# Optimization experiments

Hardware: AMD Instinct MI355X
Metric: run time of the kernel (lower is better)

The kernel has to match this reference:

```python
import jax, jax.numpy as jnp
import numpy as np

N = 50000      # num vertices
M = 10000      # num hyperedges
NNZ = 1600000  # incidence list length (avg degree 32)
D = 128        # in_features == out_features


def setup_inputs() -> dict:
    key = jax.random.key(0)
    k0, k1, k2, k3, k4, k5 = jax.random.split(key, 6)
    X = jax.random.normal(k0, (N, D), dtype=jnp.float32)
    X0 = jax.random.normal(k1, (N, D), dtype=jnp.float32)
    vertex = jax.random.randint(k2, (NNZ,), 0, N)
    edges = jax.random.randint(k3, (NNZ,), 0, M)
    # nn.Linear(D, D, bias=False) weight, kaiming-uniform-ish scale
    W = jax.random.uniform(k4, (D, D), dtype=jnp.float32,
                           minval=-1.0, maxval=1.0) / np.float32(np.sqrt(D))
    alpha = jax.random.uniform(k5, (), dtype=jnp.float32)
    beta = jnp.float32(0.5)
    return {"X": X, "X0": X0, "W": W, "alpha": alpha, "beta": beta,
            "vertex": vertex, "edges": edges}


def _scatter_mean(vals, idx, num_segments):
    # segment mean; empty segments -> 0 (matches torch_scatter 'mean')
    s = jax.ops.segment_sum(vals, idx, num_segments=num_segments)
    cnt = jax.ops.segment_sum(jnp.ones(idx.shape, vals.dtype), idx,
                              num_segments=num_segments)
    return s / jnp.maximum(cnt, 1.0)[:, None]


def reference(X, X0, W, alpha, beta, vertex, edges):
    Xve = X[vertex]                          # [NNZ, D] gather vertex -> incidence
    Xe = _scatter_mean(Xve, edges, M)        # [M, D]   hyperedge features
    Xev = Xe[edges]                          # [NNZ, D] gather edge -> incidence
    Xv = _scatter_mean(Xev, vertex, N)       # [N, D]   back to vertices
    Xi = (1.0 - alpha) * Xv + alpha * X0     # initial-residual mix
    return (1.0 - beta) * Xi + beta * (Xi @ W.T)  # identity-map mix + linear
```

## Files before the change

kernel.cpp:

```cpp
#include <hip/hip_runtime.h>
#include <hip/hip_bf16.h>


#define DD 128
#define NV 50000
#define ME 10000

#define CHUNK 4096
#define NEB 157
#define NVB 196
#define PB_CAP 12288

typedef __hip_bfloat16 bf16;
typedef __attribute__((ext_vector_type(8))) short short8v;
typedef __attribute__((ext_vector_type(4))) float float4v;

#define OFF_XE    0
#define OFF_ELIST 2560000
#define OFF_VLIST 8960000
#define OFF_EPAIR 15360000
#define OFF_VPAIR 21760000
#define OFF_XB    15360000
#define OFF_VOFF  28160000
#define OFF_EOFF  28360064
#define OFF_CBH   28400128
#define OFF_GBE   28401664
#define OFF_GBV   28402304
#define OFF_GCE   28403136
#define OFF_GCV   28403776
#define OFF_FLAG  28404608
#define OFF_WF    28404624
#define WS_USED   28470160

__device__ __forceinline__ float bf2f(unsigned short s) {
    union { unsigned u; float f; } x; x.u = ((unsigned)s) << 16; return x.f;
}
__device__ __forceinline__ unsigned f2bfu(float x) {
    union { bf16 h; unsigned short u; } c; c.h = __float2bfloat16(x); return (unsigned)c.u;
}
__device__ __forceinline__ float loadf(const void* p, long long i, unsigned f32) {
    if (f32) return ((const float*)p)[i];
    return bf2f(((const unsigned short*)p)[i]);
}
__device__ __forceinline__ float u2f_lo(unsigned x) {
    union { unsigned u; float f; } c; c.u = x << 16; return c.f;
}
__device__ __forceinline__ float u2f_hi(unsigned x) {
    union { unsigned u; float f; } c; c.u = x & 0xFFFF0000u; return c.f;
}
__device__ __forceinline__ void acc8(const uint4& u, float* a) {
    a[0] += u2f_lo(u.x); a[1] += u2f_hi(u.x);
    a[2] += u2f_lo(u.y); a[3] += u2f_hi(u.y);
    a[4] += u2f_lo(u.z); a[5] += u2f_hi(u.z);
    a[6] += u2f_lo(u.w); a[7] += u2f_hi(u.w);
}

__device__ __forceinline__ unsigned wave_is_fp32(const unsigned short* p) {
    int l = threadIdx.x & 63;
    int big = 0;
    for (int i = l; i < 256; i += 64) {
        unsigned e = (p[i] >> 7) & 0xFFu;
        if (e >= 0x90u) big++;
    }
    for (int s = 32; s > 0; s >>= 1) big += __shfl_down(big, s);
    return (__shfl(big, 0) >= 4) ? 1u : 0u;
}

__global__ __launch_bounds__(256) void prep_all(const void* X, const void* X0, const void* W,
                                                const void* beta_p,
                                                const int* __restrict__ vertex,
                                                const int* __restrict__ edges,
                                                unsigned* __restrict__ flags,
                                                unsigned short* __restrict__ Wfrag,
                                                unsigned* __restrict__ cbh, int nnz) {
    __shared__ unsigned h[NEB + NVB];
    int b = blockIdx.x, t = threadIdx.x;

    if (b == 0) {
        if (t < 64) {
            const unsigned short* px[3] = {(const unsigned short*)X,
                                           (const unsigned short*)X0,
                                           (const unsigned short*)W};
            for (int k = 0; k < 3; k++) {
                int big = 0;
                for (int i = t; i < 256; i += 64) {
                    unsigned e = (px[k][i] >> 7) & 0xFFu;
                    if (e >= 0x90u) big++;
                }
                for (int s = 32; s > 0; s >>= 1) big += __shfl_down(big, s);
                if (t == 0) flags[k] = (big >= 4) ? 1u : 0u;
            }
            if (t == 0) {
                unsigned short bb = *(const unsigned short*)beta_p;
                flags[3] = (bb == 0x3F00u) ? 0u : 1u;
            }
        }
        return;
    }

    if (b <= 8) {
        int blob = (b - 1) * 256 + t;
        unsigned fW = wave_is_fp32((const unsigned short*)W);
        unsigned short bu = *(const unsigned short*)beta_p;
        unsigned fS = (bu == 0x3F00u) ? 0u : 1u;
        int lane = blob & 63, kk = (blob >> 6) & 3, ct = blob >> 8;
        int nn = lane & 15, quad = lane >> 4;
        int c = ct * 16 + nn;
        int kbase = kk * 32 + quad * 8;
        float beta = loadf(beta_p, 0, fS);
        float omb = 1.f - beta;
        unsigned short hi[8], lo[8];
#pragma unroll
        for (int j = 0; j < 8; j++) {
            float wv = loadf(W, (long long)c * DD + kbase + j, fW);
            float v = beta * wv + ((kbase + j) == c ? omb : 0.f);
            unsigned short hh = (unsigned short)f2bfu(v);
            hi[j] = hh;
            lo[j] = (unsigned short)f2bfu(v - bf2f(hh));
        }
        uint4 ph, pl;
        ph.x = (unsigned)hi[0] | ((unsigned)hi[1] << 16);
        ph.y = (unsigned)hi[2] | ((unsigned)hi[3] << 16);
        ph.z = (unsigned)hi[4] | ((unsigned)hi[5] << 16);
        ph.w = (unsigned)hi[6] | ((unsigned)hi[7] << 16);
        pl.x = (unsigned)lo[0] | ((unsigned)lo[1] << 16);
        pl.y = (unsigned)lo[2] | ((unsigned)lo[3] << 16);
        pl.z = (unsigned)lo[4] | ((unsigned)lo[5] << 16);
        pl.w = (unsigned)lo[6] | ((unsigned)lo[7] << 16);
        ((uint4*)Wfrag)[blob] = ph;
        ((uint4*)Wfrag)[2048 + blob] = pl;
        return;
    }

    int hb = b - 9;
    for (int i = t; i < NEB + NVB; i += 256) h[i] = 0;
    __syncthreads();
    int stride = 512 * 256;
    for (int i = hb * 256 + t; i < nnz; i += stride) {
        atomicAdd(&h[edges[i] >> 6], 1u);
        atomicAdd(&h[NEB + (vertex[i] >> 8)], 1u);
    }
    __syncthreads();
    for (int i = t; i < NEB + NVB; i += 256) {
        unsigned v = h[i];
        if (v) atomicAdd(&cbh[i], v);
    }
}

__global__ __launch_bounds__(256) void conv_x(const void* __restrict__ X,
                                              unsigned short* __restrict__ Xb,
                                              const unsigned* __restrict__ flags) {
    if (!flags[0]) return;
    int i = blockIdx.x * 256 + threadIdx.x;
    if (i >= NV * DD / 8) return;
    const float4* p = (const float4*)X + (size_t)i * 2;
    float4 a = p[0], b = p[1];
    uint4 o;
    o.x = f2bfu(a.x) | (f2bfu(a.y) << 16);
    o.y = f2bfu(a.z) | (f2bfu(a.w) << 16);
    o.z = f2bfu(b.x) | (f2bfu(b.y) << 16);
    o.w = f2bfu(b.z) | (f2bfu(b.w) << 16);
    ((uint4*)Xb)[i] = o;
}

__global__ void scan353(const unsigned* __restrict__ cbh,
                        unsigned* __restrict__ gbe, unsigned* __restrict__ gbv,
                        unsigned* __restrict__ gce, unsigned* __restrict__ gcv,
                        unsigned* __restrict__ voff, unsigned* __restrict__ eoff,
                        int nnz) {
    __shared__ unsigned s[512];
    int t = threadIdx.x;
    unsigned v = (t < NEB + NVB) ? cbh[t] : 0u;
    s[t] = v;
    __syncthreads();
    for (int st = 1; st < 512; st <<= 1) {
        unsigned u = (t >= st) ? s[t - st] : 0u;
        __syncthreads();
        s[t] += u;
        __syncthreads();
    }
    unsigned excl = s[t] - v;
    if (t < NEB) {
        gbe[t] = excl; gce[t] = excl;
    } else if (t < NEB + NVB) {
        unsigned base = s[NEB - 1];
        gbv[t - NEB] = excl - base;
        gcv[t - NEB] = excl - base;
    }
    if (t == 0) {
        gbe[NEB] = (unsigned)nnz;
        gbv[NVB] = (unsigned)nnz;
        eoff[ME] = (unsigned)nnz;
        voff[NV] = (unsigned)nnz;
    }
}

__global__ __launch_bounds__(256) void build_pairs(const int* __restrict__ vertex,
                                                   const int* __restrict__ edges,
                                                   unsigned* __restrict__ gcur_e,
                                                   unsigned* __restrict__ gcur_v,
                                                   unsigned* __restrict__ epairs,
                                                   unsigned* __restrict__ vpairs, int nnz) {
    __shared__ unsigned buf[CHUNK];
    __shared__ unsigned hist[256], scn[256], loff[256], cur[256], gbase[256];
    int t = threadIdx.x;
    int base = blockIdx.x * CHUNK;
    int len = min(CHUNK, nnz - base);
    if (len <= 0) return;

    unsigned pkr[16];

    hist[t] = 0;
    __syncthreads();
#pragma unroll
    for (int it = 0; it < 16; it++) {
        int i = t + it * 256;
        if (i < len) {
            unsigned e = (unsigned)edges[base + i];
            unsigned v = (unsigned)vertex[base + i];
            unsigned pk = (e << 16) | v;
            pkr[it] = pk;
            atomicAdd(&hist[pk >> 22], 1u);
        }
    }
    __syncthreads();
    unsigned hv = hist[t];
    scn[t] = hv;
    __syncthreads();
    for (int st = 1; st < 256; st <<= 1) {
        unsigned u = (t >= st) ? scn[t - st] : 0u;
        __syncthreads();
        scn[t] += u;
        __syncthreads();
    }
    loff[t] = scn[t] - hv;
    cur[t] = scn[t] - hv;
    if (t < NEB && hv > 0) gbase[t] = atomicAdd(&gcur_e[t], hv);
    __syncthreads();
#pragma unroll
    for (int it = 0; it < 16; it++) {
        int i = t + it * 256;
        if (i < len) {
            unsigned pk = pkr[it];
            unsigned p = atomicAdd(&cur[pk >> 22], 1u);
            buf[p] = pk;
        }
    }
    __syncthreads();
    for (int i = t; i < len; i += 256) {
        unsigned pk = buf[i];
        unsigned b = pk >> 22;
        epairs[gbase[b] + (i - loff[b])] = pk;
    }

    __syncthreads();
    hist[t] = 0;
    __syncthreads();
#pragma unroll
    for (int it = 0; it < 16; it++) {
        int i = t + it * 256;
        if (i < len) {
            unsigned pk = buf[i];
            unsigned npk = (pk << 16) | (pk >> 16);
            pkr[it] = npk;
            atomicAdd(&hist[npk >> 24], 1u);
        }
    }
    __syncthreads();
    hv = hist[t];
    scn[t] = hv;
    __syncthreads();
    for (int st = 1; st < 256; st <<= 1) {
        unsigned u = (t >= st) ? scn[t - st] : 0u;
        __syncthreads();
        scn[t] += u;
        __syncthreads();
    }
    loff[t] = scn[t] - hv;
    cur[t] = scn[t] - hv;
    if (t < NVB && hv > 0) gbase[t] = atomicAdd(&gcur_v[t], hv);
    __syncthreads();
#pragma unroll
    for (int it = 0; it < 16; it++) {
        int i = t + it * 256;
        if (i < len) {
            unsigned npk = pkr[it];
            unsigned p = atomicAdd(&cur[npk >> 24], 1u);
            buf[p] = npk;
        }
    }
    __syncthreads();
    for (int i = t; i < len; i += 256) {
        unsigned npk = buf[i];
        unsigned b = npk >> 24;
        vpairs[gbase[b] + (i - loff[b])] = npk;
    }
}

__global__ __launch_bounds__(256) void build_lists(const unsigned* __restrict__ epairs,
                                                   const unsigned* __restrict__ vpairs,
                                                   const unsigned* __restrict__ gbe,
                                                   const unsigned* __restrict__ gbv,
                                                   unsigned* __restrict__ eoff,
                                                   unsigned* __restrict__ voff,
                                                   unsigned* __restrict__ elist,
                                                   unsigned* __restrict__ vlist) {
    __shared__ unsigned buf[PB_CAP];
    __shared__ unsigned offs[256], curs[256];
    int b = blockIdx.x, t = threadIdx.x;
    const unsigned* pairs;
    unsigned* off;
    unsigned* list;
    unsigned s0, s1;
    int k0, nk;
    if (b < NEB) {
        pairs = epairs; off = eoff; list = elist;
        k0 = b << 6; nk = min(64, ME - k0);
        s0 = gbe[b]; s1 = gbe[b + 1];
    } else {
        int bb = b - NEB;
        pairs = vpairs; off = voff; list = vlist;
        k0 = bb << 8; nk = min(256, NV - k0);
        s0 = gbv[bb]; s1 = gbv[bb + 1];
    }
    int len = (int)(s1 - s0);

    curs[t] = 0;
    __syncthreads();
    for (int i = t; i < len; i += 256) {
        unsigned pk = pairs[s0 + i];
        atomicAdd(&curs[(pk >> 16) - k0], 1u);
    }
    __syncthreads();
    unsigned hv = curs[t];
    offs[t] = hv;
    __syncthreads();
    for (int st = 1; st < 256; st <<= 1) {
        unsigned u = (t >= st) ? offs[t - st] : 0u;
        __syncthreads();
        offs[t] += u;
        __syncthreads();
    }
    unsigned my_excl = offs[t] - hv;
    __syncthreads();
    offs[t] = my_excl;
    curs[t] = 0;
    if (t < nk) off[k0 + t] = s0 + my_excl;
    __syncthreads();

    if (len <= PB_CAP) {
        for (int i = t; i < len; i += 256) {
            unsigned pk = pairs[s0 + i];
            int lk = (int)(pk >> 16) - k0;
            unsigned p = offs[lk] + atomicAdd(&curs[lk], 1u);
            buf[p] = pk & 0xFFFFu;
        }
        __syncthreads();
        for (int i = t; i < len; i += 256) list[s0 + i] = buf[i];
    } else {
        for (int i = t; i < len; i += 256) {
            unsigned pk = pairs[s0 + i];
            int lk = (int)(pk >> 16) - k0;
            unsigned p = offs[lk] + atomicAdd(&curs[lk], 1u);
            list[s0 + p] = pk & 0xFFFFu;
        }
    }
}

__global__ __launch_bounds__(256, 8) void edge_agg(const void* __restrict__ X,
                                                   const unsigned short* __restrict__ Xb,
                                                   const unsigned* __restrict__ eoff,
                                                   const unsigned* __restrict__ elist,
                                                   unsigned short* __restrict__ Xe,
                                                   const unsigned* __restrict__ flags, int m) {
    __shared__ float red[4][DD];
    int e = blockIdx.x;
    int t = threadIdx.x, lane = t & 63, w = t >> 6;
    const unsigned short* Xp = flags[0] ? Xb : (const unsigned short*)X;
    unsigned s0 = eoff[e], s1 = eoff[e + 1];
    float a[8];
#pragma unroll
    for (int i = 0; i < 8; i++) a[i] = 0.f;

    int sub = t & 15;
    unsigned q = s0 + (unsigned)(t >> 4);
    for (; q + 48 < s1; q += 64) {
        unsigned v0 = elist[q], v1 = elist[q + 16];
        unsigned v2 = elist[q + 32], v3 = elist[q + 48];
        uint4 u0 = *(const uint4*)(Xp + (size_t)v0 * DD + 8 * sub);
        uint4 u1 = *(const uint4*)(Xp + (size_t)v1 * DD + 8 * sub);
        uint4 u2 = *(const uint4*)(Xp + (size_t)v2 * DD + 8 * sub);
        uint4 u3 = *(const uint4*)(Xp + (size_t)v3 * DD + 8 * sub);
        acc8(u0, a); acc8(u1, a); acc8(u2, a); acc8(u3, a);
    }
    for (; q + 16 < s1; q += 32) {
        unsigned v0 = elist[q], v1 = elist[q + 16];
        uint4 u0 = *(const uint4*)(Xp + (size_t)v0 * DD + 8 * sub);
        uint4 u1 = *(const uint4*)(Xp + (size_t)v1 * DD + 8 * sub);
        acc8(u0, a); acc8(u1, a);
    }
    if (q < s1) {
        unsigned v0 = elist[q];
        uint4 u0 = *(const uint4*)(Xp + (size_t)v0 * DD + 8 * sub);
        acc8(u0, a);
    }
#pragma unroll
    for (int i = 0; i < 8; i++) {
        a[i] += __shfl_xor(a[i], 16);
        a[i] += __shfl_xor(a[i], 32);
    }
    if ((lane >> 4) == 0) {
#pragma unroll
        for (int i = 0; i < 8; i++) red[w][8 * sub + i] = a[i];
    }
    __syncthreads();
    if (t < DD) {
        float inv = (s1 > s0) ? 1.f / (float)(s1 - s0) : 1.f;
        float v = (red[0][t] + red[1][t] + red[2][t] + red[3][t]) * inv;
        Xe[(size_t)e * DD + t] = (unsigned short)f2bfu(v);
    }
}

__global__ __launch_bounds__(256, 8) void vertex_out(const unsigned short* __restrict__ Xe,
                                                     const unsigned* __restrict__ voff,
                                                     const unsigned* __restrict__ vlist,
                                                     const void* __restrict__ X0,
                                                     const unsigned short* __restrict__ Wfrag,
                                                     const void* __restrict__ alpha_p,
                                                     void* __restrict__ out,
                                                     const unsigned* __restrict__ flags, int n) {
    __shared__ short8v A_hi[272];
    __shared__ short8v A_lo[272];
    int t = threadIdx.x, lane = t & 63, w = t >> 6;
    unsigned fX = flags[0], f0 = flags[1], fS = flags[3];
    float alpha = loadf(alpha_p, 0, fS);
    float oma = 1.f - alpha;
    int v0 = blockIdx.x * 16;

    int g = lane >> 4, sub = lane & 15;
    for (int j = 0; j < 4; j++) {
        int r = w * 4 + j, v = v0 + r;
        int idx = (sub >> 2) * 68 + (sub & 3) * 17 + r;
        float a[8];
#pragma unroll
        for (int i = 0; i < 8; i++) a[i] = 0.f;
        if (v < n) {
            unsigned s0 = voff[v], s1 = voff[v + 1];
            unsigned q = s0;
            for (; q + 8 <= s1; q += 8) {
                unsigned e0 = vlist[q + g];
                unsigned e1 = vlist[q + 4 + g];
                uint4 u0 = *(const uint4*)(Xe + (size_t)e0 * DD + 8 * sub);
                uint4 u1 = *(const uint4*)(Xe + (size_t)e1 * DD + 8 * sub);
                acc8(u0, a); acc8(u1, a);
            }
            if (q + 4 <= s1) {
                unsigned e0 = vlist[q + g];
                uint4 u0 = *(const uint4*)(Xe + (size_t)e0 * DD + 8 * sub);
                acc8(u0, a);
                q += 4;
            }
            int rem = (int)(s1 - q);
            if (g < rem) {
                unsigned e0 = vlist[q + g];
                uint4 u0 = *(const uint4*)(Xe + (size_t)e0 * DD + 8 * sub);
                acc8(u0, a);
            }
#pragma unroll
            for (int i = 0; i < 8; i++) {
                a[i] += __shfl_xor(a[i], 16);
                a[i] += __shfl_xor(a[i], 32);
            }
            if (g == 0) {
                float inv = (s1 > s0) ? 1.f / (float)(s1 - s0) : 1.f;
                float x0[8];
                if (!f0) {
                    uint4 xu = *(const uint4*)((const unsigned short*)X0 + (size_t)v * DD + 8 * sub);
                    x0[0] = u2f_lo(xu.x); x0[1] = u2f_hi(xu.x);
                    x0[2] = u2f_lo(xu.y); x0[3] = u2f_hi(xu.y);
                    x0[4] = u2f_lo(xu.z); x0[5] = u2f_hi(xu.z);
                    x0[6] = u2f_lo(xu.w); x0[7] = u2f_hi(xu.w);
                } else {
                    const float4* p = (const float4*)((const float*)X0 + (size_t)v * DD + 8 * sub);
                    float4 xA = p[0], xB = p[1];
                    x0[0] = xA.x; x0[1] = xA.y; x0[2] = xA.z; x0[3] = xA.w;
                    x0[4] = xB.x; x0[5] = xB.y; x0[6] = xB.z; x0[7] = xB.w;
                }
                short8v ah, al;
#pragma unroll
                for (int i = 0; i < 8; i++) {
                    float xi = oma * (a[i] * inv) + alpha * x0[i];
                    unsigned short hh = (unsigned short)f2bfu(xi);
                    ah[i] = (short)hh;
                    al[i] = (short)f2bfu(xi - bf2f(hh));
                }
                A_hi[idx] = ah;
                A_lo[idx] = al;
            }
        } else if (g == 0) {
            short8v zf = {0, 0, 0, 0, 0, 0, 0, 0};
            A_hi[idx] = zf;
            A_lo[idx] = zf;
        }
    }

    __syncthreads();
    int ct = w;
    short8v ah[4], al[4];
#pragma unroll
    for (int kk = 0; kk < 4; kk++) {
        int ridx = kk * 68 + (lane >> 4) * 17 + (lane & 15);
        ah[kk] = A_hi[ridx];
        al[kk] = A_lo[ridx];
    }
    const short8v* Bh = (const short8v*)Wfrag;
    const short8v* Bl = Bh + 2048;
#pragma unroll
    for (int tt = 0; tt < 2; tt++) {
        int c2 = ct + 4 * tt;
        float4v acc = {0.f, 0.f, 0.f, 0.f};
#pragma unroll
        for (int kk = 0; kk < 4; kk++) {
            short8v bh = Bh[(c2 * 4 + kk) * 64 + lane];
            short8v bl = Bl[(c2 * 4 + kk) * 64 + lane];
            acc = __builtin_amdgcn_mfma_f32_16x16x32_bf16(ah[kk], bh, acc, 0, 0, 0);
            acc = __builtin_amdgcn_mfma_f32_16x16x32_bf16(al[kk], bh, acc, 0, 0, 0);
            acc = __builtin_amdgcn_mfma_f32_16x16x32_bf16(ah[kk], bl, acc, 0, 0, 0);
        }
        int col = c2 * 16 + (lane & 15);
        int rbase = v0 + (lane >> 4) * 4;
#pragma unroll
        for (int reg = 0; reg < 4; reg++) {
            int row = rbase + reg;
            if (row < n) {
                if (fX) ((float*)out)[(size_t)row * DD + col] = acc[reg];
                else    ((bf16*)out)[(size_t)row * DD + col] = __float2bfloat16(acc[reg]);
            }
        }
    }
}

extern "C" void kernel_launch(void* const* d_in, const int* in_sizes, int n_in,
                              void* d_out, int out_size, void* d_ws, size_t ws_size,
                              hipStream_t stream) {
    const void* X      = d_in[0];
    const void* X0     = d_in[1];
    const void* W      = d_in[2];
    const void* alpha  = d_in[3];
    const void* beta   = d_in[4];
    const int*  vertex = (const int*)d_in[5];
    const int*  edges  = (const int*)d_in[6];
    const int nnz = in_sizes[5];

    char* ws = (char*)d_ws;
    unsigned short* Xe = (unsigned short*)(ws + OFF_XE);
    unsigned* elist  = (unsigned*)(ws + OFF_ELIST);
    unsigned* vlist  = (unsigned*)(ws + OFF_VLIST);
    unsigned* epairs = (unsigned*)(ws + OFF_EPAIR);
    unsigned* vpairs = (unsigned*)(ws + OFF_VPAIR);
    unsigned short* Xb = (unsigned short*)(ws + OFF_XB);
    unsigned* voff   = (unsigned*)(ws + OFF_VOFF);
    unsigned* eoff   = (unsigned*)(ws + OFF_EOFF);
    unsigned* cbh    = (unsigned*)(ws + OFF_CBH);
    unsigned* gbe    = (unsigned*)(ws + OFF_GBE);
    unsigned* gbv    = (unsigned*)(ws + OFF_GBV);
    unsigned* gce    = (unsigned*)(ws + OFF_GCE);
    unsigned* gcv    = (unsigned*)(ws + OFF_GCV);
    unsigned* flags  = (unsigned*)(ws + OFF_FLAG);
    unsigned short* Wfrag = (unsigned short*)(ws + OFF_WF);

    hipMemsetAsync(ws + OFF_CBH, 0, 1536, stream);

    prep_all<<<521, 256, 0, stream>>>(X, X0, W, beta, vertex, edges,
                                      flags, Wfrag, cbh, nnz);

    scan353<<<1, 512, 0, stream>>>(cbh, gbe, gbv, gce, gcv, voff, eoff, nnz);

    int pa_blocks = (nnz + CHUNK - 1) / CHUNK;
    build_pairs<<<pa_blocks, 256, 0, stream>>>(vertex, edges, gce, gcv,
                                               epairs, vpairs, nnz);

    build_lists<<<NEB + NVB, 256, 0, stream>>>(epairs, vpairs, gbe, gbv,
                                               eoff, voff, elist, vlist);

    conv_x<<<(NV * DD / 8 + 255) / 256, 256, 0, stream>>>(X, Xb, flags);

    edge_agg<<<ME, 256, 0, stream>>>(X, Xb, eoff, elist, Xe, flags, ME);

    vertex_out<<<(NV + 15) / 16, 256, 0, stream>>>(Xe, voff, vlist, X0, Wfrag,
                                                   alpha, d_out, flags, NV);
}
```

Baseline: 265.0 us.

## Stage vertex incidence lists and X0 rows in LDS, use nontemporal loads/stores

vertex_out now copies each block's 16-vertex slice of vlist and the matching X0 rows into shared memory up front, with coalesced nontemporal loads. The gather loop then reads edge indices from LDS and unrolls to four Xe rows per step. Index-stream loads in edge_agg and the output stores are marked nontemporal so they do not pollute cache needed for the Xe/X gathers. The extra shared memory (about 12KB) leads to lowering launch bounds occupancy from 8 to 6, which could reduce latency hiding.

```diff
diff --git a/kernel.cpp b/kernel.cpp
--- a/kernel.cpp
+++ b/kernel.cpp
@@ -14,6 +14,7 @@
 typedef __hip_bfloat16 bf16;
 typedef __attribute__((ext_vector_type(8))) short short8v;
 typedef __attribute__((ext_vector_type(4))) float float4v;
+typedef __attribute__((ext_vector_type(4))) unsigned uint4v;
 
 #define OFF_XE    0
 #define OFF_ELIST 2560000
@@ -385,8 +386,10 @@
     int sub = t & 15;
     unsigned q = s0 + (unsigned)(t >> 4);
     for (; q + 48 < s1; q += 64) {
-        unsigned v0 = elist[q], v1 = elist[q + 16];
-        unsigned v2 = elist[q + 32], v3 = elist[q + 48];
+        unsigned v0 = __builtin_nontemporal_load(elist + q);
+        unsigned v1 = __builtin_nontemporal_load(elist + q + 16);
+        unsigned v2 = __builtin_nontemporal_load(elist + q + 32);
+        unsigned v3 = __builtin_nontemporal_load(elist + q + 48);
         uint4 u0 = *(const uint4*)(Xp + (size_t)v0 * DD + 8 * sub);
         uint4 u1 = *(const uint4*)(Xp + (size_t)v1 * DD + 8 * sub);
         uint4 u2 = *(const uint4*)(Xp + (size_t)v2 * DD + 8 * sub);
@@ -394,13 +397,14 @@
         acc8(u0, a); acc8(u1, a); acc8(u2, a); acc8(u3, a);
     }
     for (; q + 16 < s1; q += 32) {
-        unsigned v0 = elist[q], v1 = elist[q + 16];
+        unsigned v0 = __builtin_nontemporal_load(elist + q);
+        unsigned v1 = __builtin_nontemporal_load(elist + q + 16);
         uint4 u0 = *(const uint4*)(Xp + (size_t)v0 * DD + 8 * sub);
         uint4 u1 = *(const uint4*)(Xp + (size_t)v1 * DD + 8 * sub);
         acc8(u0, a); acc8(u1, a);
     }
     if (q < s1) {
-        unsigned v0 = elist[q];
+        unsigned v0 = __builtin_nontemporal_load(elist + q);
         uint4 u0 = *(const uint4*)(Xp + (size_t)v0 * DD + 8 * sub);
         acc8(u0, a);
     }
@@ -421,7 +425,7 @@
     }
 }
 
-__global__ __launch_bounds__(256, 8) void vertex_out(const unsigned short* __restrict__ Xe,
+__global__ __launch_bounds__(256, 6) void vertex_out(const unsigned short* __restrict__ Xe,
                                                      const unsigned* __restrict__ voff,
                                                      const unsigned* __restrict__ vlist,
                                                      const void* __restrict__ X0,
@@ -431,11 +435,46 @@
                                                      const unsigned* __restrict__ flags, int n) {
     __shared__ short8v A_hi[272];
     __shared__ short8v A_lo[272];
+    __shared__ float x0s[2048];
+    __shared__ unsigned vidx[1024];
+    __shared__ unsigned voffs[17];
     int t = threadIdx.x, lane = t & 63, w = t >> 6;
     unsigned fX = flags[0], f0 = flags[1], fS = flags[3];
     float alpha = loadf(alpha_p, 0, fS);
     float oma = 1.f - alpha;
     int v0 = blockIdx.x * 16;
+    int nv = min(16, n - v0);
+
+    if (t <= 16) voffs[t] = voff[min(v0 + t, n)];
+    __syncthreads();
+    unsigned sBase = voffs[0];
+    int tot = (int)(voffs[16] - sBase);
+    bool staged = tot <= 1024;
+
+    if (staged) {
+        for (int i = t; i < tot; i += 256)
+            vidx[i] = __builtin_nontemporal_load(vlist + sBase + i);
+    }
+    if (!f0) {
+        int cnt = nv * 16;
+        const uint4v* P = (const uint4v*)((const unsigned short*)X0 + (size_t)v0 * DD);
+        for (int i = t; i < cnt; i += 256) {
+            uint4v u = __builtin_nontemporal_load(P + i);
+            float* d = &x0s[i * 8];
+            d[0] = u2f_lo(u.x); d[1] = u2f_hi(u.x);
+            d[2] = u2f_lo(u.y); d[3] = u2f_hi(u.y);
+            d[4] = u2f_lo(u.z); d[5] = u2f_hi(u.z);
+            d[6] = u2f_lo(u.w); d[7] = u2f_hi(u.w);
+        }
+    } else {
+        int cnt = nv * 32;
+        const float4v* P = (const float4v*)((const float*)X0 + (size_t)v0 * DD);
+        for (int i = t; i < cnt; i += 256) {
+            float4v u = __builtin_nontemporal_load(P + i);
+            *((float4v*)&x0s[i * 4]) = u;
+        }
+    }
+    __syncthreads();
 
     int g = lane >> 4, sub = lane & 15;
     for (int j = 0; j < 4; j++) {
@@ -445,26 +484,47 @@
 #pragma unroll
         for (int i = 0; i < 8; i++) a[i] = 0.f;
         if (v < n) {
-            unsigned s0 = voff[v], s1 = voff[v + 1];
-            unsigned q = s0;
-            for (; q + 8 <= s1; q += 8) {
-                unsigned e0 = vlist[q + g];
-                unsigned e1 = vlist[q + 4 + g];
-                uint4 u0 = *(const uint4*)(Xe + (size_t)e0 * DD + 8 * sub);
-                uint4 u1 = *(const uint4*)(Xe + (size_t)e1 * DD + 8 * sub);
-                acc8(u0, a); acc8(u1, a);
-            }
-            if (q + 4 <= s1) {
-                unsigned e0 = vlist[q + g];
-                uint4 u0 = *(const uint4*)(Xe + (size_t)e0 * DD + 8 * sub);
-                acc8(u0, a);
-                q += 4;
-            }
-            int rem = (int)(s1 - q);
-            if (g < rem) {
-                unsigned e0 = vlist[q + g];
-                uint4 u0 = *(const uint4*)(Xe + (size_t)e0 * DD + 8 * sub);
-                acc8(u0, a);
+            unsigned ls0 = voffs[r] - sBase, ls1 = voffs[r + 1] - sBase;
+            unsigned q = ls0;
+            if (staged) {
+                for (; q + 16 <= ls1; q += 16) {
+                    unsigned e0 = vidx[q + g], e1 = vidx[q + 4 + g];
+                    unsigned e2 = vidx[q + 8 + g], e3 = vidx[q + 12 + g];
+                    uint4 u0 = *(const uint4*)(Xe + (size_t)e0 * DD + 8 * sub);
+                    uint4 u1 = *(const uint4*)(Xe + (size_t)e1 * DD + 8 * sub);
+                    uint4 u2 = *(const uint4*)(Xe + (size_t)e2 * DD + 8 * sub);
+                    uint4 u3 = *(const uint4*)(Xe + (size_t)e3 * DD + 8 * sub);
+                    acc8(u0, a); acc8(u1, a); acc8(u2, a); acc8(u3, a);
+                }
+                for (; q + 4 <= ls1; q += 4) {
+                    unsigned e0 = vidx[q + g];
+                    uint4 u0 = *(const uint4*)(Xe + (size_t)e0 * DD + 8 * sub);
+                    acc8(u0, a);
+                }
+                if (g < (int)(ls1 - q)) {
+                    unsigned e0 = vidx[q + g];
+                    uint4 u0 = *(const uint4*)(Xe + (size_t)e0 * DD + 8 * sub);
+                    acc8(u0, a);
+                }
+            } else {
+                const unsigned* vp = vlist + sBase;
+                for (; q + 8 <= ls1; q += 8) {
+                    unsigned e0 = __builtin_nontemporal_load(vp + q + g);
+                    unsigned e1 = __builtin_nontemporal_load(vp + q + 4 + g);
+                    uint4 u0 = *(const uint4*)(Xe + (size_t)e0 * DD + 8 * sub);
+                    uint4 u1 = *(const uint4*)(Xe + (size_t)e1 * DD + 8 * sub);
+                    acc8(u0, a); acc8(u1, a);
+                }
+                for (; q + 4 <= ls1; q += 4) {
+                    unsigned e0 = __builtin_nontemporal_load(vp + q + g);
+                    uint4 u0 = *(const uint4*)(Xe + (size_t)e0 * DD + 8 * sub);
+                    acc8(u0, a);
+                }
+                if (g < (int)(ls1 - q)) {
+                    unsigned e0 = __builtin_nontemporal_load(vp + q + g);
+                    uint4 u0 = *(const uint4*)(Xe + (size_t)e0 * DD + 8 * sub);
+                    acc8(u0, a);
+                }
             }
 #pragma unroll
             for (int i = 0; i < 8; i++) {
@@ -472,24 +532,13 @@
                 a[i] += __shfl_xor(a[i], 32);
             }
             if (g == 0) {
-                float inv = (s1 > s0) ? 1.f / (float)(s1 - s0) : 1.f;
-                float x0[8];
-                if (!f0) {
-                    uint4 xu = *(const uint4*)((const unsigned short*)X0 + (size_t)v * DD + 8 * sub);
-                    x0[0] = u2f_lo(xu.x); x0[1] = u2f_hi(xu.x);
-                    x0[2] = u2f_lo(xu.y); x0[3] = u2f_hi(xu.y);
-                    x0[4] = u2f_lo(xu.z); x0[5] = u2f_hi(xu.z);
-                    x0[6] = u2f_lo(xu.w); x0[7] = u2f_hi(xu.w);
-                } else {
-                    const float4* p = (const float4*)((const float*)X0 + (size_t)v * DD + 8 * sub);
-                    float4 xA = p[0], xB = p[1];
-                    x0[0] = xA.x; x0[1] = xA.y; x0[2] = xA.z; x0[3] = xA.w;
-                    x0[4] = xB.x; x0[5] = xB.y; x0[6] = xB.z; x0[7] = xB.w;
-                }
+                unsigned deg = ls1 - ls0;
+                float inv = deg ? 1.f / (float)deg : 1.f;
+                const float* xr = &x0s[r * 128 + 8 * sub];
                 short8v ah, al;
 #pragma unroll
                 for (int i = 0; i < 8; i++) {
-                    float xi = oma * (a[i] * inv) + alpha * x0[i];
+                    float xi = oma * (a[i] * inv) + alpha * xr[i];
                     unsigned short hh = (unsigned short)f2bfu(xi);
                     ah[i] = (short)hh;
                     al[i] = (short)f2bfu(xi - bf2f(hh));
@@ -533,8 +582,15 @@
         for (int reg = 0; reg < 4; reg++) {
             int row = rbase + reg;
             if (row < n) {
-                if (fX) ((float*)out)[(size_t)row * DD + col] = acc[reg];
-                else    ((bf16*)out)[(size_t)row * DD + col] = __float2bfloat16(acc[reg]);
+                if (fX) {
+                    __builtin_nontemporal_store(acc[reg],
+                        (float*)out + (size_t)row * DD + col);
+                } else {
+                    bf16 hv = __float2bfloat16(acc[reg]);
+                    unsigned short hb = *(unsigned short*)&hv;
+                    __builtin_nontemporal_store(hb,
+                        (unsigned short*)out + (size_t)row * DD + col);
+                }
             }
         }
     }
```

New measurement: 257.0 us. 1.03x faster.
